# Performance work log

Measured on AMD Instinct MI355X. Metric: run time of the kernel, lower is better.

The kernel has to match this reference:

```python
import jax, jax.numpy as jnp
import numpy as np
jax.config.update("jax_enable_x64", True)  # subchunk uses float64 decays (T=128 > 24)

B, T, D = 4, 2048, 1024
H, K = 16, 64            # head_size = 64, D = H*K
CHUNK = 128              # T % 128 == 0 -> only the 128-chunk path of _chunked_wkv runs
DMIX, DDEC = 32, 64      # D_MIX_DIM, D_DECAY_DIM
PREC_MIN = 0.005
LN_EPS = 1e-5 * 8.0 ** 2 # eps * head_size_divisor**2


def setup_inputs() -> dict:
    key = jax.random.key(0)
    ks = jax.random.split(key, 24)
    f32 = jnp.float32
    rn = lambda k, s, sc=1.0: (jax.random.normal(k, s) * sc).astype(f32)
    un = lambda k, s, lo, hi: jax.random.uniform(k, s, minval=lo, maxval=hi).astype(f32)
    inv_sq = 1.0 / np.sqrt(D)
    return {
        "x": rn(ks[0], (B, T, D)),
        # token-mix interpolation coefficients (init-like: in [0,1])
        "time_maa_x": un(ks[1], (1, 1, D), 0.0, 1.0),
        "time_maa_w": un(ks[2], (1, 1, D), 0.0, 1.0),
        "time_maa_k": un(ks[3], (1, 1, D), 0.0, 1.0),
        "time_maa_v": un(ks[4], (1, 1, D), 0.0, 1.0),
        "time_maa_r": un(ks[5], (1, 1, D), 0.0, 1.0),
        "time_maa_g": un(ks[6], (1, 1, D), 0.0, 1.0),
        "time_maa_w1": rn(ks[7], (D, 5 * DMIX), 0.01),
        "time_maa_w2": un(ks[8], (5, DMIX, D), -0.01, 0.01),
        # decay: init range roughly [-6, -1] like the module
        "time_decay": un(ks[9], (1, 1, D), -6.0, -1.0),
        "time_decay_w1": rn(ks[10], (D, DDEC), 0.01),
        "time_decay_w2": un(ks[11], (DDEC, D), -0.01, 0.01),
        "time_faaaa": un(ks[12], (H, K), -0.1, 0.5),
        # projections (stored [in, out]; x @ W == nn.Linear)
        "Wr": rn(ks[13], (D, D), inv_sq),
        "Wk": rn(ks[14], (D, D), inv_sq),
        "Wv": rn(ks[15], (D, D), inv_sq),
        "Wg": rn(ks[16], (D, D), inv_sq),
        "Wo": rn(ks[17], (D, D), inv_sq),
        "ln_w": jnp.ones((D,), f32),
        "ln_b": jnp.zeros((D,), f32),
    }


def _causal_shift(x):
    # x[t-1], zero at t=0
    return jnp.pad(x[:, :-1, :], ((0, 0), (1, 0), (0, 0)))


def _chunked_wkv(r, k, v, w, u, state):
    # r,k,v,w: [B,H,L,K]; u: [1,H,1,K]; state: [B,H,K,V]
    Bb, Hh, L, Kk = r.shape
    V = v.shape[-1]
    Tc = CHUNK
    N = L // Tc
    f64 = jnp.float64

    w_decay = jnp.clip(jnp.exp(w), PREC_MIN, None)
    wc_log = jnp.log(w_decay.astype(jnp.float32)).reshape(Bb, Hh, N, Tc, Kk)
    wc_cum = jnp.cumsum(wc_log, axis=-2)                              # inclusive cumsum over chunk
    shifted = jnp.pad(wc_cum[..., :-1, :], ((0, 0),) * 3 + ((1, 0), (0, 0)))
    ws = wc_log.sum(axis=-2, keepdims=True)                           # [B,H,N,1,K] total log-decay
    w_inter = jnp.exp(ws - wc_cum).astype(r.dtype)
    w_intra = jnp.exp(wc_cum - wc_log).astype(r.dtype)

    rc = r.reshape(Bb, Hh, N, Tc, Kk)
    kc = k.reshape(Bb, Hh, N, Tc, Kk)
    vc = v.reshape(Bb, Hh, N, Tc, V)

    # intra-chunk attention in float64 with mid-chunk offset for stability
    off = shifted[..., Tc // 2:Tc // 2 + 1, :]
    r_decay = jnp.exp((shifted - off).astype(f64))
    k_inv = jnp.exp((off - wc_cum).astype(f64))
    a = jnp.einsum('bhnik,bhnjk->bhnij', rc.astype(f64) * r_decay,
                   kc.astype(f64) * k_inv).astype(r.dtype)
    a = jnp.tril(a, -1)
    diag = jnp.einsum('bhntk,bhntk->bhnt', rc, u[:, :, :, None, :] * kc)  # u bonus on the diagonal
    a = a + diag[..., None] * jnp.eye(Tc, dtype=r.dtype)
    out = jnp.einsum('bhnij,bhnjv->bhniv', a, vc)

    # inter-chunk recurrent state carry
    wkv = jnp.einsum('bhntk,bhntv->bhnkv', kc * w_inter, vc)          # per-chunk KV update
    ws_e = jnp.swapaxes(jnp.exp(ws), -1, -2).astype(r.dtype)          # [B,H,N,K,1]

    def step(s, xs):
        wkv_i, ws_i = xs
        return s * ws_i + wkv_i, s                                    # emit state BEFORE update

    state_f, states = jax.lax.scan(step, state,
                                   (jnp.moveaxis(wkv, 2, 0), jnp.moveaxis(ws_e, 2, 0)))
    states = jnp.moveaxis(states, 0, 2)                               # [B,H,N,K,V]
    out = out + jnp.einsum('bhntk,bhnkv->bhntv', rc * w_intra, states)
    return out.reshape(Bb, Hh, L, V), state_f


def reference(x, time_maa_x, time_maa_w, time_maa_k, time_maa_v, time_maa_r,
              time_maa_g, time_maa_w1, time_maa_w2, time_decay, time_decay_w1,
              time_decay_w2, time_faaaa, Wr, Wk, Wv, Wg, Wo, ln_w, ln_b):
    Bb, Tt, Dd = x.shape
    xx = _causal_shift(x) - x                                          # dxprev (recurrent mode)

    # data-dependent 5-way token-mix (RWKV-6 LoRA mix)
    xxx = jnp.tanh((x + xx * time_maa_x) @ time_maa_w1)                # [B,T,5*DMIX]
    m = jnp.einsum('btfi,fid->fbtd', xxx.reshape(Bb, Tt, 5, DMIX), time_maa_w2)
    mw, mk, mv, mr, mg = m
    xw = x + xx * (time_maa_w + mw)
    xk = x + xx * (time_maa_k + mk)
    xv = x + xx * (time_maa_v + mv)
    xr = x + xx * (time_maa_r + mr)
    xg = x + xx * (time_maa_g + mg)

    to_heads = lambda t: t.reshape(Bb, Tt, H, K).transpose(0, 2, 1, 3)  # [B,H,T,K]
    r = to_heads(xr @ Wr)
    k = to_heads(xk @ Wk)
    v = to_heads(xv @ Wv)
    g = jax.nn.silu(xg @ Wg)

    ww = time_decay + jnp.tanh(xw @ time_decay_w1) @ time_decay_w2
    w = to_heads(-jnp.exp(ww))                                         # log-decay (negative)
    u = time_faaaa.reshape(1, H, 1, K)

    state0 = jnp.zeros((Bb, H, K, K), dtype=x.dtype)
    out, _state = _chunked_wkv(r, k, v, w, u, state0)

    # GroupNorm(n_head groups) over flattened (B*T, D)
    og = out.transpose(0, 2, 1, 3).reshape(Bb * Tt, H, K)
    mu = og.mean(-1, keepdims=True)
    var = og.var(-1, keepdims=True)
    og = (og - mu) / jnp.sqrt(var + LN_EPS)
    out = (og.reshape(Bb * Tt, Dd) * ln_w + ln_b).reshape(Bb, Tt, Dd)

    return (out * g) @ Wo
```

## Files before the change

### kernel.cpp

```cpp
#include <hip/hip_runtime.h>
#include <hip/hip_bf16.h>
#include <math.h>
#include <stdint.h>

typedef __hip_bfloat16 bf16;
typedef __attribute__((ext_vector_type(8))) short short8;
typedef __attribute__((ext_vector_type(4))) short short4v;
typedef __attribute__((ext_vector_type(4))) float f32x4;

#define Tt 2048
#define Dd 1024
#define Hh 16

__device__ __forceinline__ float b2f(bf16 v){ return __bfloat162float(v); }
__device__ __forceinline__ bf16  f2b(float v){ return __float2bfloat16(v); }

__device__ __forceinline__ void async16(const void* g, void* l){
  __builtin_amdgcn_global_load_lds(
      (__attribute__((address_space(1))) void*)(g),
      (__attribute__((address_space(3))) void*)(l),
      16, 0, 0);
}

__device__ __forceinline__ int seg_t(int lr, int t0, int Lm1){ return t0 + (lr & Lm1); }
__device__ __forceinline__ size_t seg_grow(int lr, int b0, int t0, int Llog2, int Lm1){
  return ((size_t)(b0 + (lr >> Llog2)) * Tt) + (size_t)seg_t(lr, t0, Lm1);
}

__device__ __forceinline__ void xcd_swz(int& bn, int& bm, int& z){
  int nbm = gridDim.y;
  if((nbm & 7) == 0){
    int flat = blockIdx.x + (blockIdx.y << 3) + blockIdx.z * (nbm << 3);
    int j = flat & 7, k = flat >> 3;
    int cs = nbm >> 3;
    bn = (k & 7) << 7;
    int kk = k >> 3;
    bm = (j * cs + (kk % cs)) << 7;
    z  = kk / cs;
  } else {
    bn = blockIdx.x << 7; bm = blockIdx.y << 7; z = blockIdx.z;
  }
}

__device__ __forceinline__ void xcd_swz_g(int& bn, int& bm, int& z){
  int gx = gridDim.x, gy = gridDim.y;
  if((gy & 7) == 0){
    int flat = blockIdx.x + gx * (blockIdx.y + gy * blockIdx.z);
    int j = flat & 7, k = flat >> 3;
    int cs = gy >> 3;
    int bn_t = k % gx; int kk = k / gx;
    int bm_t = j * cs + (kk % cs);
    z  = kk / cs;
    bn = bn_t << 7; bm = bm_t << 7;
  } else {
    bn = blockIdx.x << 7; bm = blockIdx.y << 7; z = blockIdx.z;
  }
}

struct MixP { const bf16* maa[5]; bf16* dst[5]; };
struct Proj4 { const bf16* A[4]; const bf16* Bt[4]; bf16* C[4]; };
struct ConvP { const void* src[20]; bf16* dst[20]; };
struct T5P  { const bf16* src[5]; bf16* dst[5]; };

__global__ __launch_bounds__(256) void k_detect(const unsigned short* __restrict__ xs,
                                                int* __restrict__ flag){
  __shared__ int bad;
  if(threadIdx.x == 0) bad = 0;
  __syncthreads();
  int local = 0;
  for(int i = threadIdx.x; i < 8192; i += 256){
    unsigned e = (xs[i] >> 7) & 0xFF;
    if(e >= 0xC0) local++;
  }
  if(local) atomicAdd(&bad, local);
  __syncthreads();
  if(threadIdx.x == 0) flag[0] = (bad > 16) ? 1 : 0;
}

__global__ __launch_bounds__(256) void k_conv_all(ConvP p, const int* __restrict__ flag){
  const int PRE[21] = {0,8388608,8389632,8390656,8391680,8392704,8393728,8394752,
                       8558592,8722432,8723456,8788992,8854528,8855552,9904128,
                       10952704,12001280,13049856,14098432,14099456,14100480};
  int v = (blockIdx.x * 256 + threadIdx.x) * 4;
  if(v >= 14100480) return;
  int a = 0;
  #pragma unroll
  for(int i = 1; i < 20; i++) if(v >= PRE[i]) a = i;
  int off = v - PRE[a];
  bf16* d = p.dst[a] + off;
  if(flag[0]){
    f32x4 xv = *(const f32x4*)((const float*)p.src[a] + off);
    short4v o;
    #pragma unroll
    for(int j = 0; j < 4; j++) ((bf16*)&o)[j] = f2b(xv[j]);
    *(short4v*)d = o;
  } else {
    *(short4v*)d = *(const short4v*)((const short*)p.src[a] + off);
  }
}

__global__ __launch_bounds__(256) void k_transpose5(T5P p){
  __shared__ bf16 tile[32][33];
  const bf16* __restrict__ src = p.src[blockIdx.z];
  bf16* __restrict__ dst       = p.dst[blockIdx.z];
  int bx = blockIdx.x * 32, by = blockIdx.y * 32;
  int tx = threadIdx.x & 31, ty = threadIdx.x >> 5;
  for(int r = ty; r < 32; r += 8)
    tile[r][tx] = src[(size_t)(by + r) * 1024 + bx + tx];
  __syncthreads();
  for(int r = ty; r < 32; r += 8)
    dst[(size_t)(bx + r) * 1024 + by + tx] = tile[tx][r];
}

__global__ __launch_bounds__(256) void k_transposeP(const bf16* __restrict__ src,
                                                    bf16* __restrict__ dst,
                                                    int K, int N, int Npad){
  int idx = blockIdx.x * 256 + threadIdx.x;
  if(idx >= Npad * K) return;
  int n = idx / K, k = idx - n * K;
  dst[idx] = (n < N) ? src[(size_t)k * N + n] : f2b(0.f);
}

__global__ __launch_bounds__(256) void k_transposeP5(const bf16* __restrict__ src,
                                                     bf16* __restrict__ dst){
  int z = blockIdx.z;
  int idx = blockIdx.x * 256 + threadIdx.x;
  int n = idx >> 5, k = idx & 31;
  dst[(size_t)z * 32768 + idx] = src[(size_t)z * 32768 + (size_t)k * 1024 + n];
}

__global__ __launch_bounds__(256) void k_prep(const bf16* __restrict__ x,
                                              const bf16* __restrict__ tmx,
                                              bf16* __restrict__ xmx,
                                              int b0, int t0, int Llog2){
  const int Lm1 = (1 << Llog2) - 1;
  int idx = blockIdx.x * 256 + threadIdx.x;
  int lr = idx >> 10, d = idx & 1023;
  size_t grow = seg_grow(lr, b0, t0, Llog2, Lm1);
  int tl = seg_t(lr, t0, Lm1);
  float xc = b2f(x[grow * Dd + d]);
  float xp = tl ? b2f(x[(grow - 1) * Dd + d]) : 0.f;
  xmx[idx] = f2b(xc + (xp - xc) * b2f(tmx[d]));
}

constexpr int GEPI_BF16 = 0, GEPI_SILU = 1, GEPI_OUT = 2;

template<int EPI>
__global__ __launch_bounds__(256) void gemm_mfma(
    const bf16* __restrict__ A,
    const bf16* __restrict__ Bt,
    void* __restrict__ Cv,
    const int* __restrict__ oflag,
    int rowoff){
  __shared__ __align__(16) short As[128 * 32];
  __shared__ __align__(16) short Bs[128 * 32];
  int tid = threadIdx.x;
  int bn, bm, zz;
  xcd_swz(bn, bm, zz);
  int w = tid >> 6, lane = tid & 63;
  int wm = (w & 1) * 64, wn = (w >> 1) * 64;
  int m16 = lane & 15, quad = lane >> 4;

  f32x4 acc[4][4];
  #pragma unroll
  for(int mi = 0; mi < 4; mi++)
    #pragma unroll
    for(int ni = 0; ni < 4; ni++)
      acc[mi][ni] = (f32x4){0.f, 0.f, 0.f, 0.f};

  int srow = tid >> 2;
  int sk8  = (tid & 3) * 8;
  const bf16* Ag = A  + (size_t)(bm + srow) * 1024 + sk8;
  const bf16* Bg = Bt + (size_t)(bn + srow) * 1024 + sk8;
  short* Al = As + w * 512;
  short* Bl = Bs + w * 512;

  for(int kb = 0; kb < 1024; kb += 32){
    #pragma unroll
    for(int rep = 0; rep < 2; rep++){
      async16(Ag + (size_t)rep * 64 * 1024 + kb, Al + rep * 2048);
      async16(Bg + (size_t)rep * 64 * 1024 + kb, Bl + rep * 2048);
    }
    __syncthreads();
    short8 af[4], bfr[4];
    #pragma unroll
    for(int mi = 0; mi < 4; mi++)
      af[mi] = *(const short8*)(As + (wm + mi * 16 + m16) * 32 + quad * 8);
    #pragma unroll
    for(int ni = 0; ni < 4; ni++)
      bfr[ni] = *(const short8*)(Bs + (wn + ni * 16 + m16) * 32 + quad * 8);
    #pragma unroll
    for(int mi = 0; mi < 4; mi++)
      #pragma unroll
      for(int ni = 0; ni < 4; ni++)
        acc[mi][ni] = __builtin_amdgcn_mfma_f32_16x16x32_bf16(af[mi], bfr[ni], acc[mi][ni], 0, 0, 0);
    __syncthreads();
  }
  #pragma unroll
  for(int mi = 0; mi < 4; mi++){
    #pragma unroll
    for(int ni = 0; ni < 4; ni++){
      #pragma unroll
      for(int r = 0; r < 4; r++){
        int row = bm + wm + mi * 16 + quad * 4 + r;
        int col = bn + wn + ni * 16 + m16;
        float v = acc[mi][ni][r];
        if constexpr(EPI == GEPI_BF16){
          ((bf16*)Cv)[(size_t)row * 1024 + col] = f2b(v);
        } else if constexpr(EPI == GEPI_SILU){
          ((bf16*)Cv)[(size_t)row * 1024 + col] = f2b(v / (1.f + expf(-v)));
        } else {
          size_t off = (size_t)(row + rowoff) * 1024 + col;
          if(oflag[0]) ((float*)Cv)[off] = v;
          else         ((bf16*)Cv)[off]  = f2b(v);
        }
      }
    }
  }
}

__global__ __launch_bounds__(512) void gemm256(Proj4 prm){
  __shared__ __align__(16) short lds3[3][16384];
  int tid = threadIdx.x;
  int flat = blockIdx.x + (blockIdx.y << 2) + (blockIdx.z << 7);
  int j = flat & 7, k = flat >> 3;
  int bn = (k & 3) << 8;
  int kk = k >> 2;
  int bm = ((j << 2) + (kk & 3)) << 8;
  int z  = kk >> 2;
  const bf16* __restrict__ A  = prm.A[z];
  const bf16* __restrict__ Bt = prm.Bt[z];
  bf16* __restrict__ C        = prm.C[z];
  int w = tid >> 6, lane = tid & 63;
  int wm = (w & 1) * 128, wn = (w >> 1) * 64;
  int m16 = lane & 15, quad = lane >> 4;

  f32x4 acc[8][4];
  #pragma unroll
  for(int mi = 0; mi < 8; mi++)
    #pragma unroll
    for(int ni = 0; ni < 4; ni++)
      acc[mi][ni] = (f32x4){0.f, 0.f, 0.f, 0.f};

  int srow = tid >> 2;
  int c4   = ((tid & 3) - (srow >> 1)) & 3;
  const bf16* Ag = A  + (size_t)(bm + srow) * 1024 + c4 * 8;
  const bf16* Bg = Bt + (size_t)(bn + srow) * 1024 + c4 * 8;

  auto STG = [&](int buf, int t){
    int kb = t << 5;
    #pragma unroll
    for(int rep = 0; rep < 2; rep++){
      async16(Ag + (size_t)rep * 128 * 1024 + kb, &lds3[buf][rep * 4096 + w * 512]);
      async16(Bg + (size_t)rep * 128 * 1024 + kb, &lds3[buf][8192 + rep * 4096 + w * 512]);
    }
  };
  STG(0, 0); STG(1, 1);
  asm volatile("s_waitcnt vmcnt(4)" ::: "memory");
  __builtin_amdgcn_s_barrier();
  __builtin_amdgcn_sched_barrier(0);

  #pragma unroll
  for(int t = 0; t < 32; t++){
    const int bufR = t % 3;
    const int bufS = (t + 2) % 3;
    if(t + 2 < 32) STG(bufS, t + 2);
    const short* As_b = &lds3[bufR][0];
    const short* Bs_b = &lds3[bufR][8192];
    short8 af[8], bfr[4];
    #pragma unroll
    for(int mi = 0; mi < 8; mi++){
      int ar = wm + mi * 16 + m16;
      af[mi] = *(const short8*)(As_b + ar * 32 + ((quad + (ar >> 1)) & 3) * 8);
    }
    #pragma unroll
    for(int ni = 0; ni < 4; ni++){
      int br = wn + ni * 16 + m16;
      bfr[ni] = *(const short8*)(Bs_b + br * 32 + ((quad + (br >> 1)) & 3) * 8);
    }
    __builtin_amdgcn_s_setprio(1);
    #pragma unroll
    for(int mi = 0; mi < 8; mi++)
      #pragma unroll
      for(int ni = 0; ni < 4; ni++)
        acc[mi][ni] = __builtin_amdgcn_mfma_f32_16x16x32_bf16(af[mi], bfr[ni], acc[mi][ni], 0, 0, 0);
    __builtin_amdgcn_s_setprio(0);
    __builtin_amdgcn_sched_barrier(0);
    if(t + 2 < 32){
      asm volatile("s_waitcnt vmcnt(4)" ::: "memory");
    } else if(t + 2 == 32){
      asm volatile("s_waitcnt vmcnt(0)" ::: "memory");
    }
    if(t < 31){
      __builtin_amdgcn_s_barrier();
      __builtin_amdgcn_sched_barrier(0);
    }
  }
  bool silu = (z == 3);
  #pragma unroll
  for(int mi = 0; mi < 8; mi++){
    #pragma unroll
    for(int ni = 0; ni < 4; ni++){
      #pragma unroll
      for(int r = 0; r < 4; r++){
        int row = bm + wm + mi * 16 + quad * 4 + r;
        int col = bn + wn + ni * 16 + m16;
        float v = acc[mi][ni][r];
        if(silu) v = v / (1.f + expf(-v));
        C[(size_t)row * 1024 + col] = f2b(v);
      }
    }
  }
}

__global__ __launch_bounds__(256) void gemm_mix(
    const bf16* __restrict__ xxx,
    const bf16* __restrict__ w2T,
    const bf16* __restrict__ xg,
    MixP prm, int b0, int t0, int Llog2){
  const int Lm1 = (1 << Llog2) - 1;
  __shared__ __align__(16) short As[128 * 32];
  __shared__ __align__(16) short Bs[128 * 32];
  int tid = threadIdx.x;
  int bn, bm, c;
  xcd_swz_g(bn, bm, c);
  int w = tid >> 6, lane = tid & 63;
  int wm = (w & 1) * 64, wn = (w >> 1) * 64;
  int m16 = lane & 15, quad = lane >> 4;

  int srow = tid >> 2;
  int sk8  = (tid & 3) * 8;
  short* Al = As + w * 512;
  short* Bl = Bs + w * 512;
  #pragma unroll
  for(int rep = 0; rep < 2; rep++){
    async16(xxx + (size_t)(bm + srow + rep * 64) * 256 + c * 32 + sk8, Al + rep * 2048);
    async16(w2T + (size_t)c * 32768 + (size_t)(bn + srow + rep * 64) * 32 + sk8, Bl + rep * 2048);
  }
  __syncthreads();
  f32x4 acc[4][4];
  short8 af[4], bfr[4];
  #pragma unroll
  for(int mi = 0; mi < 4; mi++)
    af[mi] = *(const short8*)(As + (wm + mi * 16 + m16) * 32 + quad * 8);
  #pragma unroll
  for(int ni = 0; ni < 4; ni++)
    bfr[ni] = *(const short8*)(Bs + (wn + ni * 16 + m16) * 32 + quad * 8);
  #pragma unroll
  for(int mi = 0; mi < 4; mi++)
    #pragma unroll
    for(int ni = 0; ni < 4; ni++)
      acc[mi][ni] = __builtin_amdgcn_mfma_f32_16x16x32_bf16(
          af[mi], bfr[ni], (f32x4){0.f, 0.f, 0.f, 0.f}, 0, 0, 0);

  const bf16* maa = prm.maa[c];
  bf16* dst = prm.dst[c];
  #pragma unroll
  for(int mi = 0; mi < 4; mi++){
    #pragma unroll
    for(int ni = 0; ni < 4; ni++){
      #pragma unroll
      for(int r = 0; r < 4; r++){
        int row = bm + wm + mi * 16 + quad * 4 + r;
        int col = bn + wn + ni * 16 + m16;
        size_t grow = seg_grow(row, b0, t0, Llog2, Lm1);
        int tl = seg_t(row, t0, Lm1);
        float xc = b2f(xg[grow * Dd + col]);
        float xp = tl ? b2f(xg[(grow - 1) * Dd + col]) : 0.f;
        dst[(size_t)row * 1024 + col] =
            f2b(xc + (xp - xc) * (b2f(maa[col]) + acc[mi][ni][r]));
      }
    }
  }
}

constexpr int G2_TANH = 0, G2_DECAY = 1;

template<int EPI>
__global__ __launch_bounds__(256) void gemm_mfma2(
    const bf16* __restrict__ A,
    const bf16* __restrict__ Bt,
    void* __restrict__ Cv, int ldc,
    int Ndim, int Kdim,
    const bf16* __restrict__ e_w){
  __shared__ __align__(16) short As[128 * 32];
  __shared__ __align__(16) short Bs[128 * 32];
  int tid = threadIdx.x;
  int bn, bm, zz;
  xcd_swz_g(bn, bm, zz);
  int w = tid >> 6, lane = tid & 63;
  int wm = (w & 1) * 64, wn = (w >> 1) * 64;
  int m16 = lane & 15, quad = lane >> 4;

  f32x4 acc[4][4];
  #pragma unroll
  for(int mi = 0; mi < 4; mi++)
    #pragma unroll
    for(int ni = 0; ni < 4; ni++)
      acc[mi][ni] = (f32x4){0.f, 0.f, 0.f, 0.f};

  int srow = tid >> 2;
  int sk8  = (tid & 3) * 8;
  const bf16* Ag = A  + (size_t)(bm + srow) * Kdim + sk8;
  const bf16* Bg = Bt + (size_t)(bn + srow) * Kdim + sk8;
  short* Al = As + w * 512;
  short* Bl = Bs + w * 512;

  for(int kb = 0; kb < Kdim; kb += 32){
    #pragma unroll
    for(int rep = 0; rep < 2; rep++){
      async16(Ag + (size_t)rep * 64 * Kdim + kb, Al + rep * 2048);
      async16(Bg + (size_t)rep * 64 * Kdim + kb, Bl + rep * 2048);
    }
    __syncthreads();
    short8 af[4], bfr[4];
    #pragma unroll
    for(int mi = 0; mi < 4; mi++)
      af[mi] = *(const short8*)(As + (wm + mi * 16 + m16) * 32 + quad * 8);
    #pragma unroll
    for(int ni = 0; ni < 4; ni++)
      bfr[ni] = *(const short8*)(Bs + (wn + ni * 16 + m16) * 32 + quad * 8);
    #pragma unroll
    for(int mi = 0; mi < 4; mi++)
      #pragma unroll
      for(int ni = 0; ni < 4; ni++)
        acc[mi][ni] = __builtin_amdgcn_mfma_f32_16x16x32_bf16(af[mi], bfr[ni], acc[mi][ni], 0, 0, 0);
    __syncthreads();
  }
  #pragma unroll
  for(int mi = 0; mi < 4; mi++){
    #pragma unroll
    for(int ni = 0; ni < 4; ni++){
      #pragma unroll
      for(int r = 0; r < 4; r++){
        int row = bm + wm + mi * 16 + quad * 4 + r;
        int col = bn + wn + ni * 16 + m16;
        if(col >= Ndim) continue;
        float v = acc[mi][ni][r];
        size_t off = (size_t)row * ldc + col;
        if constexpr(EPI == G2_TANH){
          ((bf16*)Cv)[off] = f2b(tanhf(v));
        } else {
          float td = b2f(e_w[col]) + v;
          ((float*)Cv)[off] = fmaxf(-expf(td), -5.2983173665480363f);
        }
      }
    }
  }
}

constexpr int EPI_OUTV = 5;
#define BM 64
#define BN 64
#define BK 16

template<int EPI>
__global__ __launch_bounds__(256) void gemm_ep(
    const bf16* __restrict__ A, int lda,
    const bf16* __restrict__ Bm, int ldb,
    void* __restrict__ Cv, int ldc,
    int Mdim, int Ndim, int Kdim,
    const bf16* __restrict__ xg, const bf16* __restrict__ e_w,
    int b0, int t0, int Llog2, const int* __restrict__ oflag){
  const int Lm1 = (1 << Llog2) - 1;
  __shared__ float As[BM][BK + 1];
  __shared__ float Bs[BK][BN + 4];
  int tid = threadIdx.x;
  int tx = tid & 15, ty = tid >> 4;
  int bm = blockIdx.y * BM, bn = blockIdx.x * BN;
  float acc[4][4] = {};
  for(int kb = 0; kb < Kdim; kb += BK){
    {
      int lr = tid >> 2;
      int lc = (tid & 3) * 4;
      int gr = bm + lr;
      #pragma unroll
      for(int q = 0; q < 4; q++){
        int gc = kb + lc + q;
        float av = 0.f;
        if(gr < Mdim && gc < Kdim)
          av = b2f(A[(size_t)gr * lda + gc]);
        As[lr][lc + q] = av;
      }
    }
    {
      int lr = tid >> 4;
      int lc = (tid & 15) * 4;
      #pragma unroll
      for(int q = 0; q < 4; q++){
        int gr = kb + lr; int gc = bn + lc + q;
        Bs[lr][lc + q] = (gr < Kdim && gc < Ndim) ? b2f(Bm[(size_t)gr * ldb + gc]) : 0.f;
      }
    }
    __syncthreads();
    #pragma unroll
    for(int kk = 0; kk < BK; kk++){
      float ar[4], br[4];
      #pragma unroll
      for(int q = 0; q < 4; q++) ar[q] = As[ty * 4 + q][kk];
      #pragma unroll
      for(int q = 0; q < 4; q++) br[q] = Bs[kk][tx * 4 + q];
      #pragma unroll
      for(int mi = 0; mi < 4; mi++)
        #pragma unroll
        for(int ni = 0; ni < 4; ni++)
          acc[mi][ni] += ar[mi] * br[ni];
    }
    __syncthreads();
  }
  #pragma unroll
  for(int mi = 0; mi < 4; mi++){
    int row = bm + ty * 4 + mi;
    if(row >= Mdim) continue;
    #pragma unroll
    for(int ni = 0; ni < 4; ni++){
      int col = bn + tx * 4 + ni;
      if(col >= Ndim) continue;
      float vacc = acc[mi][ni];
      size_t grow = seg_grow(row, b0, t0, Llog2, Lm1);
      size_t go = grow * Dd + col;
      if(oflag[0]) ((float*)Cv)[go] = vacc;
      else         ((bf16*)Cv)[go]  = f2b(vacc);
    }
  }
}

__global__ __launch_bounds__(256) void k_cumsum(float* __restrict__ wd,
                                                float* __restrict__ wse,
                                                int nlog2){
  int blk = blockIdx.x;
  int dg = blk & 3; int rest = blk >> 2;
  int nmask = (1 << nlog2) - 1;
  int ln = rest & nmask; int bp = rest >> nlog2;
  int d = dg * 256 + threadIdx.x;
  size_t rowbase = (((size_t)bp << nlog2) + ln) * 128;
  size_t base = rowbase * Dd + d;
  float c = 0.f;
  for(int t = 0; t < 128; t++){
    size_t ix = base + (size_t)t * Dd;
    c += wd[ix];
    wd[ix] = c;
  }
  int h = d >> 6, k0 = d & 63;
  wse[((((size_t)bp * Hh + h) << nlog2) | ln) * 64 + k0] = __expf(fminf(c, 0.f));
}

__global__ __launch_bounds__(256) void k_chunk1(const bf16* __restrict__ kb,
                                                const bf16* __restrict__ vb,
                                                const float* __restrict__ wcum,
                                                float* __restrict__ wkv,
                                                int nlog2){
  __shared__ __align__(16) bf16 ktT[64 * 136];
  __shared__ __align__(16) bf16 vT2[64 * 136];
  int tid = threadIdx.x, blk = blockIdx.x;
  int nmask = (1 << nlog2) - 1;
  int ln = blk & nmask; int rest = blk >> nlog2;
  int h = rest & 15; int bp = rest >> 4;
  size_t rowbase = (((size_t)bp << nlog2) + ln) * 128;
  size_t gbase = rowbase * Dd + h * 64;
  for(int r = 0; r < 32; r++){
    int idx = r * 256 + tid;
    int t0 = idx >> 6, k0 = idx & 63;
    size_t gi = gbase + (size_t)t0 * Dd + k0;
    float c  = wcum[gi];
    float cL = wcum[gbase + (size_t)127 * Dd + k0];
    ktT[k0 * 136 + t0] = f2b(b2f(kb[gi]) * __expf(fminf(cL - c, 0.f)));
    vT2[k0 * 136 + t0] = vb[gi];
  }
  __syncthreads();
  int w = tid >> 6, lane = tid & 63;
  int m16 = lane & 15, quad = lane >> 4;
  f32x4 acc[4];
  #pragma unroll
  for(int nt = 0; nt < 4; nt++) acc[nt] = (f32x4){0.f, 0.f, 0.f, 0.f};
  #pragma unroll
  for(int ks = 0; ks < 4; ks++){
    short8 af = *(const short8*)(ktT + (w * 16 + m16) * 136 + ks * 32 + quad * 8);
    #pragma unroll
    for(int nt = 0; nt < 4; nt++){
      short8 bfr = *(const short8*)(vT2 + (nt * 16 + m16) * 136 + ks * 32 + quad * 8);
      acc[nt] = __builtin_amdgcn_mfma_f32_16x16x32_bf16(af, bfr, acc[nt], 0, 0, 0);
    }
  }
  size_t obase = (size_t)blk * 4096;
  #pragma unroll
  for(int nt = 0; nt < 4; nt++)
    #pragma unroll
    for(int r = 0; r < 4; r++)
      wkv[obase + (size_t)(w * 16 + quad * 4 + r) * 64 + nt * 16 + m16] = acc[nt][r];
}

__global__ __launch_bounds__(256) void k_scan(float* __restrict__ buf,
                                              const float* __restrict__ wse,
                                              float* __restrict__ st,
                                              int b0, int firstseg, int nlog2){
  int blk = blockIdx.x;
  int h = blk & 15, bp = blk >> 4;
  int tid = threadIdx.x;
  size_t stbase = ((size_t)(b0 + bp) * Hh + h) * 4096;
  int nloc = 1 << nlog2;
  float s[16];
  #pragma unroll
  for(int r = 0; r < 16; r++)
    s[r] = firstseg ? 0.f : st[stbase + r * 256 + tid];
  for(int ln = 0; ln < nloc; ln++){
    size_t idx = (((size_t)bp * Hh + h) << nlog2) | ln;
    size_t base = idx * 4096;
    const float* wsp = wse + idx * 64;
    #pragma unroll
    for(int r = 0; r < 16; r++){
      int e = r * 256 + tid;
      float tmp = buf[base + e];
      buf[base + e] = s[r];
      s[r] = s[r] * wsp[e >> 6] + tmp;
    }
  }
  #pragma unroll
  for(int r = 0; r < 16; r++)
    st[stbase + r * 256 + tid] = s[r];
}

__global__ __launch_bounds__(256) void k_chunk2(
    const bf16* __restrict__ rb, const bf16* __restrict__ kb,
    const bf16* __restrict__ vb, const float* __restrict__ wcum,
    const float* __restrict__ states, const bf16* __restrict__ u,
    float* __restrict__ outw, int nlog2){
  __shared__ __align__(16) bf16 vT[64 * 136];
  __shared__ __align__(16) bf16 sT[64 * 72];
  __shared__ __align__(16) bf16 ascr[4 * 16 * 136];
  int tid = threadIdx.x, blk = blockIdx.x;
  int nmask = (1 << nlog2) - 1;
  int ln = blk & nmask; int rest = blk >> nlog2;
  int h = rest & 15; int bp = rest >> 4;
  size_t rowbase = (((size_t)bp << nlog2) + ln) * 128;
  size_t gbase = rowbase * Dd + h * 64;
  for(int r = 0; r < 32; r++){
    int idx = r * 256 + tid;
    int t0 = idx >> 6, v0 = idx & 63;
    vT[v0 * 136 + t0] = vb[gbase + (size_t)t0 * Dd + v0];
  }
  for(int r = 0; r < 16; r++){
    int idx = r * 256 + tid;
    int k0 = idx >> 6, v0 = idx & 63;
    sT[v0 * 72 + k0] = f2b(states[(size_t)blk * 4096 + k0 * 64 + v0]);
  }
  __syncthreads();
  int w = tid >> 6, lane = tid & 63;
  int m16 = lane & 15, quad = lane >> 4;
  bf16* scr = ascr + w * (16 * 136);
  f32x4 oacc[2][4];
  #pragma unroll
  for(int a1 = 0; a1 < 2; a1++)
    #pragma unroll
    for(int a2 = 0; a2 < 4; a2++) oacc[a1][a2] = (f32x4){0.f, 0.f, 0.f, 0.f};

  for(int ii = 0; ii < 2; ii++){
    int I = ii ? (7 - w) : w;
    int B = I * 16;
    for(int z = lane; z < 544; z += 64) ((unsigned long long*)scr)[z] = 0ULL;
    int i0 = B + m16;
    size_t rowi = rowbase + i0;
    short8 rf[2], af[2], rw2[2];
    float crv[2][8];
    #pragma unroll
    for(int ks = 0; ks < 2; ks++){
      int koff = h * 64 + ks * 32 + quad * 8;
      rf[ks] = *(const short8*)(rb + rowi * Dd + koff);
      float cp[8];
      if(i0 > 0){
        f32x4 c0 = *(const f32x4*)(wcum + (rowi - 1) * Dd + koff);
        f32x4 c1 = *(const f32x4*)(wcum + (rowi - 1) * Dd + koff + 4);
        #pragma unroll
        for(int c = 0; c < 4; c++){ cp[c] = c0[c]; cp[4 + c] = c1[c]; }
      } else {
        #pragma unroll
        for(int c = 0; c < 8; c++) cp[c] = 0.f;
      }
      if(B > 0){
        f32x4 c0 = *(const f32x4*)(wcum + (rowbase + B - 1) * Dd + koff);
        f32x4 c1 = *(const f32x4*)(wcum + (rowbase + B - 1) * Dd + koff + 4);
        #pragma unroll
        for(int c = 0; c < 4; c++){ crv[ks][c] = c0[c]; crv[ks][4 + c] = c1[c]; }
      } else {
        #pragma unroll
        for(int c = 0; c < 8; c++) crv[ks][c] = 0.f;
      }
      short8 av, wv;
      #pragma unroll
      for(int c = 0; c < 8; c++){
        float rv = b2f(((const bf16*)&rf[ks])[c]);
        ((bf16*)&av)[c] = f2b(rv * __expf(fminf(cp[c] - crv[ks][c], 0.f)));
        ((bf16*)&wv)[c] = f2b(rv * __expf(fminf(cp[c], 0.f)));
      }
      af[ks] = av; rw2[ks] = wv;
    }
    for(int J = 0; J < I; J++){
      f32x4 aacc = (f32x4){0.f, 0.f, 0.f, 0.f};
      #pragma unroll
      for(int ks = 0; ks < 2; ks++){
        int koff = h * 64 + ks * 32 + quad * 8;
        size_t rowj = rowbase + J * 16 + m16;
        short8 k8 = *(const short8*)(kb + rowj * Dd + koff);
        f32x4 c0 = *(const f32x4*)(wcum + rowj * Dd + koff);
        f32x4 c1 = *(const f32x4*)(wcum + rowj * Dd + koff + 4);
        short8 bfrag;
        #pragma unroll
        for(int c = 0; c < 8; c++){
          float kv = b2f(((const bf16*)&k8)[c]);
          float cj = (c < 4) ? c0[c] : c1[c - 4];
          ((bf16*)&bfrag)[c] = f2b(kv * __expf(fminf(crv[ks][c] - cj, 0.f)));
        }
        aacc = __builtin_amdgcn_mfma_f32_16x16x32_bf16(af[ks], bfrag, aacc, 0, 0, 0);
      }
      #pragma unroll
      for(int r = 0; r < 4; r++)
        scr[(quad * 4 + r) * 136 + J * 16 + m16] = f2b(aacc[r]);
    }
    {
      f32x4 aacc = (f32x4){0.f, 0.f, 0.f, 0.f};
      f32x4 dacc = (f32x4){0.f, 0.f, 0.f, 0.f};
      #pragma unroll
      for(int ks = 0; ks < 2; ks++){
        int koff = h * 64 + ks * 32 + quad * 8;
        size_t rowj = rowbase + B + m16;
        short8 k8 = *(const short8*)(kb + rowj * Dd + koff);
        f32x4 c0 = *(const f32x4*)(wcum + rowj * Dd + koff);
        f32x4 c1 = *(const f32x4*)(wcum + rowj * Dd + koff + 4);
        short8 u8 = *(const short8*)(u + h * 64 + ks * 32 + quad * 8);
        short8 bf1, bf2;
        #pragma unroll
        for(int c = 0; c < 8; c++){
          float kv = b2f(((const bf16*)&k8)[c]);
          float cj = (c < 4) ? c0[c] : c1[c - 4];
          ((bf16*)&bf1)[c] = f2b(kv * __expf(crv[ks][c] - cj));
          ((bf16*)&bf2)[c] = f2b(kv * b2f(((const bf16*)&u8)[c]));
        }
        aacc = __builtin_amdgcn_mfma_f32_16x16x32_bf16(af[ks], bf1, aacc, 0, 0, 0);
        dacc = __builtin_amdgcn_mfma_f32_16x16x32_bf16(rf[ks], bf2, dacc, 0, 0, 0);
      }
      #pragma unroll
      for(int r = 0; r < 4; r++){
        int row = quad * 4 + r, col = m16;
        if(col < row)       scr[row * 136 + B + col] = f2b(aacc[r]);
        else if(col == row) scr[row * 136 + B + col] = f2b(dacc[r]);
      }
    }
    asm volatile("s_waitcnt lgkmcnt(0)" ::: "memory");
    int nks = (I + 2) >> 1;
    for(int ks2 = 0; ks2 < nks; ks2++){
      short8 afr = *(const short8*)(scr + m16 * 136 + ks2 * 32 + quad * 8);
      #pragma unroll
      for(int nt = 0; nt < 4; nt++){
        short8 bfr = *(const short8*)(vT + (nt * 16 + m16) * 136 + ks2 * 32 + quad * 8);
        oacc[ii][nt] = __builtin_amdgcn_mfma_f32_16x16x32_bf16(afr, bfr, oacc[ii][nt], 0, 0, 0);
      }
    }
    #pragma unroll
    for(int ks = 0; ks < 2; ks++){
      #pragma unroll
      for(int nt = 0; nt < 4; nt++){
        short8 sfr = *(const short8*)(sT + (nt * 16 + m16) * 72 + ks * 32 + quad * 8);
        oacc[ii][nt] = __builtin_amdgcn_mfma_f32_16x16x32_bf16(rw2[ks], sfr, oacc[ii][nt], 0, 0, 0);
      }
    }
  }
  __syncthreads();
  #pragma unroll
  for(int ii = 0; ii < 2; ii++){
    int I = ii ? (7 - w) : w;
    int B = I * 16;
    #pragma unroll
    for(int nt = 0; nt < 4; nt++){
      #pragma unroll
      for(int r = 0; r < 4; r++){
        int i0 = B + quad * 4 + r;
        int v0 = nt * 16 + m16;
        outw[gbase + (size_t)i0 * Dd + v0] = oacc[ii][nt][r];
      }
    }
  }
}

__global__ __launch_bounds__(256) void k_norm(const float* __restrict__ outw,
                                              const bf16* __restrict__ gb,
                                              const bf16* __restrict__ lnw,
                                              const bf16* __restrict__ lnb,
                                              bf16* __restrict__ gated){
  int lr = blockIdx.x;
  int wv = threadIdx.x >> 6, lane = threadIdx.x & 63;
  for(int hh = wv; hh < Hh; hh += 4){
    size_t ix = (size_t)lr * Dd + hh * 64 + lane;
    float xv = outw[ix];
    float s1 = xv, s2 = xv * xv;
    #pragma unroll
    for(int off = 32; off > 0; off >>= 1){
      s1 += __shfl_xor(s1, off);
      s2 += __shfl_xor(s2, off);
    }
    float mu  = s1 * 0.015625f;
    float var = s2 * 0.015625f - mu * mu;
    float inv = rsqrtf(var + 6.4e-4f);
    float og  = (xv - mu) * inv * b2f(lnw[hh * 64 + lane]) + b2f(lnb[hh * 64 + lane]);
    gated[ix] = f2b(og * b2f(gb[ix]));
  }
}

extern "C" void kernel_launch(void* const* d_in, const int* in_sizes, int n_in,
                              void* d_out, int out_size, void* d_ws, size_t ws_size,
                              hipStream_t stream){
  char* W = (char*)d_ws;
  size_t cur = 0;
  auto carve = [&](size_t bytes) -> char* {
    char* p = W + cur;
    cur = (cur + bytes + 255) & ~(size_t)255;
    return p;
  };

  int* flag = (int*)carve(4096);
  static const int NEL[20] = {8388608, 1024, 1024, 1024, 1024, 1024, 1024,
                              163840, 163840, 1024, 65536, 65536, 1024,
                              1048576, 1048576, 1048576, 1048576, 1048576,
                              1024, 1024};
  bf16* canon[20];
  for(int i = 0; i < 20; i++) canon[i] = (bf16*)carve((size_t)NEL[i] * 2);

  k_detect<<<dim3(1), 256, 0, stream>>>((const unsigned short*)d_in[0], flag);
  ConvP cp;
  for(int i = 0; i < 20; i++){ cp.src[i] = d_in[i]; cp.dst[i] = canon[i]; }
  k_conv_all<<<dim3(13770), 256, 0, stream>>>(cp, flag);

  const bf16* xp   = canon[0];
  const bf16* tmx  = canon[1];
  const bf16* tdec = canon[9];
  const bf16* up   = canon[12];
  const bf16* lnwp = canon[18];
  const bf16* lnbp = canon[19];

  bf16* WrT  = (bf16*)carve(2097152);
  bf16* WkT  = (bf16*)carve(2097152);
  bf16* WvT  = (bf16*)carve(2097152);
  bf16* WgT  = (bf16*)carve(2097152);
  bf16* WoT  = (bf16*)carve(2097152);
  bf16* W1T  = (bf16*)carve(256 * 1024 * 2);
  bf16* DW1T = (bf16*)carve(128 * 1024 * 2);
  bf16* DW2T = (bf16*)carve(1024 * 64 * 2);
  bf16* W2T  = (bf16*)carve(5 * 1024 * 32 * 2);
  T5P tp;
  tp.src[0] = canon[13]; tp.dst[0] = WrT;
  tp.src[1] = canon[14]; tp.dst[1] = WkT;
  tp.src[2] = canon[15]; tp.dst[2] = WvT;
  tp.src[3] = canon[16]; tp.dst[3] = WgT;
  tp.src[4] = canon[17]; tp.dst[4] = WoT;
  k_transpose5<<<dim3(32, 32, 5), 256, 0, stream>>>(tp);
  k_transposeP<<<dim3(1024), 256, 0, stream>>>(canon[7],  W1T,  1024, 160, 256);
  k_transposeP<<<dim3(512),  256, 0, stream>>>(canon[10], DW1T, 1024, 64, 128);
  k_transposeP<<<dim3(256),  256, 0, stream>>>(canon[11], DW2T, 64, 1024, 1024);
  k_transposeP5<<<dim3(128, 1, 5), 256, 0, stream>>>(canon[8], W2T);

  float* st = (float*)carve(1u << 20);
  size_t FIXED = cur;

  const size_t UNIT = 19104, PAD = 65536;
  int nb, L;
  if(ws_size >= FIXED + (size_t)8192 * UNIT + PAD){ nb = 4; L = 2048; }
  else {
    nb = 1; L = 2048;
    while(L > 128 && ws_size < FIXED + (size_t)L * UNIT + PAD) L >>= 1;
  }
  const int Llog2 = __builtin_ctz((unsigned)L);
  const int nlog2 = Llog2 - 7;
  const int M     = nb * L;
  const size_t Mr = (size_t)M;

  bf16*  xxx    = (bf16*) carve(Mr * 512);
  bf16*  ww1    = (bf16*) carve(Mr * 128);
  float* wse    = (float*)carve(Mr * 32);
  bf16*  xmx    = (bf16*) carve(Mr * 2048);
  bf16*  mixbuf = (bf16*) carve(Mr * 2048);
  bf16*  kbuf   = (bf16*) carve(Mr * 2048);
  bf16*  vbuf   = (bf16*) carve(Mr * 2048);
  bf16*  rbuf   = (bf16*) carve(Mr * 2048);
  bf16*  gbuf   = (bf16*) carve(Mr * 2048);
  float* wdec   = (float*)carve(Mr * 4096);
  float* wkvst  = (float*)carve(Mr * 2048);
  float* outw   = wdec;
  bf16*  gated  = mixbuf;

  MixP mp;
  mp.maa[0] = canon[2]; mp.maa[1] = canon[3]; mp.maa[2] = canon[4];
  mp.maa[3] = canon[5]; mp.maa[4] = canon[6];
  mp.dst[0] = mixbuf;
  mp.dst[1] = (bf16*)wdec;
  mp.dst[2] = (bf16*)wdec + Mr * 1024;
  mp.dst[3] = (bf16*)wkvst;
  mp.dst[4] = xmx;

  Proj4 pp;
  pp.A[0] = mp.dst[1]; pp.Bt[0] = WkT; pp.C[0] = kbuf;
  pp.A[1] = mp.dst[2]; pp.Bt[1] = WvT; pp.C[1] = vbuf;
  pp.A[2] = mp.dst[3]; pp.Bt[2] = WrT; pp.C[2] = rbuf;
  pp.A[3] = mp.dst[4]; pp.Bt[3] = WgT; pp.C[3] = gbuf;

  for(int b0 = 0; b0 < 4; b0 += nb){
    for(int t0 = 0; t0 < Tt; t0 += L){
      k_prep<<<dim3(M * 4), 256, 0, stream>>>(xp, tmx, xmx, b0, t0, Llog2);
      gemm_mfma2<G2_TANH><<<dim3(2, M/128), 256, 0, stream>>>(
          xmx, W1T, xxx, 256, 160, 1024, nullptr);
      gemm_mix<<<dim3(8, M/128, 5), 256, 0, stream>>>(
          xxx, W2T, xp, mp, b0, t0, Llog2);
      if(M == 8192){
        gemm256<<<dim3(4, 32, 4), 512, 0, stream>>>(pp);
      } else {
        for(int z = 0; z < 4; z++){
          if(z == 3)
            gemm_mfma<GEPI_SILU><<<dim3(8, M/128), 256, 0, stream>>>(pp.A[z], pp.Bt[z], pp.C[z], flag, 0);
          else
            gemm_mfma<GEPI_BF16><<<dim3(8, M/128), 256, 0, stream>>>(pp.A[z], pp.Bt[z], pp.C[z], flag, 0);
        }
      }
      gemm_mfma2<G2_TANH><<<dim3(1, M/128), 256, 0, stream>>>(
          mixbuf, DW1T, ww1, 64, 64, 1024, nullptr);
      gemm_mfma2<G2_DECAY><<<dim3(8, M/128), 256, 0, stream>>>(
          ww1, DW2T, wdec, 1024, 1024, 64, tdec);
      int nloc = 1 << nlog2;
      k_cumsum<<<dim3(nb * nloc * 4), 256, 0, stream>>>(wdec, wse, nlog2);
      k_chunk1<<<dim3(nb * 16 * nloc), 256, 0, stream>>>(kbuf, vbuf, wdec, wkvst, nlog2);
      k_scan<<<dim3(nb * 16), 256, 0, stream>>>(wkvst, wse, st, b0, (t0 == 0) ? 1 : 0, nlog2);
      k_chunk2<<<dim3(nb * 16 * nloc), 256, 0, stream>>>(rbuf, kbuf, vbuf, wdec, wkvst, up, outw, nlog2);
      k_norm<<<dim3(M), 256, 0, stream>>>(outw, gbuf, lnwp, lnbp, gated);
      if(L == Tt){
        gemm_mfma<GEPI_OUT><<<dim3(8, M/128), 256, 0, stream>>>(gated, WoT, d_out, flag, b0 * Tt);
      } else {
        gemm_ep<EPI_OUTV><<<dim3(16, M/64), 256, 0, stream>>>(
            gated, 1024, canon[17], 1024, d_out, 1024, M, 1024, 1024,
            nullptr, nullptr, b0, t0, Llog2, flag);
      }
    }
  }
}
```

Before: 531.3 us.

## Triple-buffer GEMM LDS tiles with async prefetch and swizzled layout

```diff
diff --git a/kernel.cpp b/kernel.cpp
--- a/kernel.cpp
+++ b/kernel.cpp
@@ -152,8 +152,7 @@
     void* __restrict__ Cv,
     const int* __restrict__ oflag,
     int rowoff){
-  __shared__ __align__(16) short As[128 * 32];
-  __shared__ __align__(16) short Bs[128 * 32];
+  __shared__ __align__(16) short lds3[3][8192];
   int tid = threadIdx.x;
   int bn, bm, zz;
   xcd_swz(bn, bm, zz);
@@ -169,32 +168,58 @@
       acc[mi][ni] = (f32x4){0.f, 0.f, 0.f, 0.f};
 
   int srow = tid >> 2;
-  int sk8  = (tid & 3) * 8;
-  const bf16* Ag = A  + (size_t)(bm + srow) * 1024 + sk8;
-  const bf16* Bg = Bt + (size_t)(bn + srow) * 1024 + sk8;
-  short* Al = As + w * 512;
-  short* Bl = Bs + w * 512;
-
-  for(int kb = 0; kb < 1024; kb += 32){
+  int c4   = ((tid & 3) - (srow >> 1)) & 3;
+  const bf16* Ag = A  + (size_t)(bm + srow) * 1024 + c4 * 8;
+  const bf16* Bg = Bt + (size_t)(bn + srow) * 1024 + c4 * 8;
+
+  auto STG = [&](int buf, int t){
+    int kb = t << 5;
     #pragma unroll
     for(int rep = 0; rep < 2; rep++){
-      async16(Ag + (size_t)rep * 64 * 1024 + kb, Al + rep * 2048);
-      async16(Bg + (size_t)rep * 64 * 1024 + kb, Bl + rep * 2048);
-    }
-    __syncthreads();
+      async16(Ag + (size_t)rep * 64 * 1024 + kb, &lds3[buf][rep * 2048 + w * 512]);
+      async16(Bg + (size_t)rep * 64 * 1024 + kb, &lds3[buf][4096 + rep * 2048 + w * 512]);
+    }
+  };
+  STG(0, 0); STG(1, 1);
+  asm volatile("s_waitcnt vmcnt(4)" ::: "memory");
+  __builtin_amdgcn_s_barrier();
+  __builtin_amdgcn_sched_barrier(0);
+
+  #pragma unroll
+  for(int t = 0; t < 32; t++){
+    const int bufR = t % 3;
+    const int bufS = (t + 2) % 3;
+    if(t + 2 < 32) STG(bufS, t + 2);
+    const short* As_b = &lds3[bufR][0];
+    const short* Bs_b = &lds3[bufR][4096];
     short8 af[4], bfr[4];
     #pragma unroll
-    for(int mi = 0; mi < 4; mi++)
-      af[mi] = *(const short8*)(As + (wm + mi * 16 + m16) * 32 + quad * 8);
-    #pragma unroll
-    for(int ni = 0; ni < 4; ni++)
-      bfr[ni] = *(const short8*)(Bs + (wn + ni * 16 + m16) * 32 + quad * 8);
+    for(int mi = 0; mi < 4; mi++){
+      int ar = wm + mi * 16 + m16;
+      af[mi] = *(const short8*)(As_b + ar * 32 + ((quad + (ar >> 1)) & 3) * 8);
+    }
+    #pragma unroll
+    for(int ni = 0; ni < 4; ni++){
+      int br = wn + ni * 16 + m16;
+      bfr[ni] = *(const short8*)(Bs_b + br * 32 + ((quad + (br >> 1)) & 3) * 8);
+    }
+    __builtin_amdgcn_s_setprio(1);
     #pragma unroll
     for(int mi = 0; mi < 4; mi++)
       #pragma unroll
       for(int ni = 0; ni < 4; ni++)
         acc[mi][ni] = __builtin_amdgcn_mfma_f32_16x16x32_bf16(af[mi], bfr[ni], acc[mi][ni], 0, 0, 0);
-    __syncthreads();
+    __builtin_amdgcn_s_setprio(0);
+    __builtin_amdgcn_sched_barrier(0);
+    if(t + 2 < 32){
+      asm volatile("s_waitcnt vmcnt(4)" ::: "memory");
+    } else if(t + 2 == 32){
+      asm volatile("s_waitcnt vmcnt(0)" ::: "memory");
+    }
+    if(t < 31){
+      __builtin_amdgcn_s_barrier();
+      __builtin_amdgcn_sched_barrier(0);
+    }
   }
   #pragma unroll
   for(int mi = 0; mi < 4; mi++){
```

After: 528.2 us. Within noise of the previous version (-0.6%).
